# Optimization experiments

Measured on AMD Instinct MI355X. Metric: run time of the kernel, lower is better.

Reference implementation:

```python
import jax, jax.numpy as jnp
import numpy as np

D_MODEL = 512
NHEAD = 8


def setup_inputs() -> dict:
    key = jax.random.key(0)
    ks = jax.random.split(key, 8)
    d = D_MODEL
    low_feats = jax.random.normal(ks[0], (1, d, 32, 32), dtype=jnp.float32)
    guide_feats = jax.random.normal(ks[1], (1, d, 128, 128), dtype=jnp.float32)
    s = 1.0 / np.sqrt(d)
    Wq = jax.random.normal(ks[2], (d, d), dtype=jnp.float32) * s
    Wk = jax.random.normal(ks[3], (d, d), dtype=jnp.float32) * s
    Wv = jax.random.normal(ks[4], (d, d), dtype=jnp.float32) * s
    Wm = jax.random.normal(ks[5], (d, d), dtype=jnp.float32) * s
    gamma = jnp.ones((d,), dtype=jnp.float32)
    beta = jnp.zeros((d,), dtype=jnp.float32)
    return {"low_feats": low_feats, "guide_feats": guide_feats, "Wq": Wq,
            "Wk": Wk, "Wv": Wv, "Wm": Wm, "gamma": gamma, "beta": beta}


def _gather_windows(feat_hw, H, W):
    # feat_hw: [b, h, w, nhead, dim]. For each guide pixel (Y,X), nearest low
    # pixel is (Y*h//H, X*w//W) (PyTorch 'nearest'); gather its 3x3 neighborhood
    # with replicate padding (index clamping). Window order = ky*3+kx, matching
    # F.unfold channel layout. Returns [b, H*W, 9, nhead, dim].
    b, h, w, nh, dm = feat_hw.shape
    offs = jnp.array([-1, 0, 1])
    y0 = jnp.arange(H) * h // H                      # [H]
    x0 = jnp.arange(W) * w // W                      # [W]
    ys = jnp.clip(y0[:, None] + offs, 0, h - 1)      # [H,3] (ky)
    xs = jnp.clip(x0[:, None] + offs, 0, w - 1)      # [W,3] (kx)
    # -> [b, H, W, 3(ky), 3(kx), nhead, dim]
    g = feat_hw[:, ys[:, None, :, None], xs[None, :, None, :]]
    return g.reshape(b, H * W, 9, nh, dm)


def reference(low_feats, guide_feats, Wq, Wk, Wv, Wm, gamma, beta):
    b, d, H, W = guide_feats.shape
    _, _, h, w = low_feats.shape
    nh = NHEAD
    dm = d // nh
    g = guide_feats.transpose(0, 2, 3, 1).reshape(b, H * W, d)
    l = low_feats.transpose(0, 2, 3, 1).reshape(b, h * w, d)
    q = (g @ Wq.T).reshape(b, H * W, nh, dm)                 # [b,N,h,d]
    K = (l @ Wk.T).reshape(b, h, w, nh, dm)
    V = (l @ Wv.T).reshape(b, h, w, nh, dm)
    key = _gather_windows(K, H, W)                           # [b,N,9,h,d]
    val = _gather_windows(V, H, W)
    scale = 1.0 / jnp.sqrt(jnp.asarray(dm, dtype=q.dtype))
    # (q/sqrt(dm)) @ (k/sqrt(dm)) * sqrt(dm) == q@k / sqrt(dm)
    score = jnp.einsum('bnhd,bnkhd->bnhk', q, key) * scale
    attn = jax.nn.softmax(score, axis=-1)
    msg = jnp.einsum('bnhk,bnkhd->bnhd', attn, val).reshape(b, H * W, d)
    msg = msg @ Wm.T
    # LayerNorm(d_model), eps=1e-5
    mu = jnp.mean(msg, axis=-1, keepdims=True)
    var = jnp.mean((msg - mu) ** 2, axis=-1, keepdims=True)
    msg = (msg - mu) * jax.lax.rsqrt(var + 1e-5) * gamma + beta
    return msg.transpose(0, 2, 1).reshape(b, d, H, W)
```

## Files before the change

### kernel.cpp

```cpp
#include <hip/hip_runtime.h>
#include <hip/hip_bf16.h>
#include <stdint.h>

#define NQ 16384
#define NL 1024
#define DM 512

typedef __bf16 bf16_t;
typedef __bf16 bf16x8 __attribute__((ext_vector_type(8)));
typedef __bf16 bf16x4 __attribute__((ext_vector_type(4)));
typedef float f32x4 __attribute__((ext_vector_type(4)));

__device__ __forceinline__ void gload_lds16(const void* g, void* l) {
  __builtin_amdgcn_global_load_lds(
      (const __attribute__((address_space(1))) uint32_t*)g,
      (__attribute__((address_space(3))) uint32_t*)l, 16, 0, 0);
}

__global__ __launch_bounds__(256) void cvt_transpose(const float* __restrict__ src,
                                                     bf16_t* __restrict__ dst, int ncols) {
  __shared__ float tl[32][33];
  const int n0 = blockIdx.x * 32, c0 = blockIdx.y * 32;
  const int t = threadIdx.x, c = t & 31, r = t >> 5;
#pragma unroll
  for (int it = 0; it < 4; ++it) {
    int rr = r + it * 8;
    tl[rr][c] = src[(size_t)(c0 + rr) * ncols + n0 + c];
  }
  __syncthreads();
#pragma unroll
  for (int it = 0; it < 4; ++it) {
    int rr = r + it * 8;
    dst[(size_t)(n0 + rr) * 512 + c0 + c] = (bf16_t)tl[c][rr];
  }
}

__global__ __launch_bounds__(256) void cvt_w(const float* __restrict__ s0, const float* __restrict__ s1,
                                             const float* __restrict__ s2, const float* __restrict__ s3,
                                             bf16_t* __restrict__ d0, bf16_t* __restrict__ d1,
                                             bf16_t* __restrict__ d2, bf16_t* __restrict__ d3) {
  const float* s;
  bf16_t* d;
  switch (blockIdx.y) {
    case 0: s = s0; d = d0; break;
    case 1: s = s1; d = d1; break;
    case 2: s = s2; d = d2; break;
    default: s = s3; d = d3; break;
  }
  const int i = (blockIdx.x * 256 + threadIdx.x) * 4;
  float4 v = *(const float4*)(s + i);
  bf16x4 o = {(bf16_t)v.x, (bf16_t)v.y, (bf16_t)v.z, (bf16_t)v.w};
  *(bf16x4*)(d + i) = o;
}

template <typename OutT>
__global__ __launch_bounds__(256) void gemm_bt(const bf16_t* __restrict__ A,
                                               const bf16_t* __restrict__ B,
                                               OutT* __restrict__ C, int M, int N, int K) {
  __shared__ __align__(16) bf16_t As[128 * 64];
  __shared__ __align__(16) bf16_t Bs[128 * 64];
  const int t = threadIdx.x;
  const int lane = t & 63;
  const int wave = t >> 6;
  const int wr = (wave >> 1) * 64;
  const int wc = (wave & 1) * 64;
  const int bm = blockIdx.x * 128;
  const int bn = blockIdx.y * 128;
  const int r0 = t >> 3;
  const int c0 = (t & 7) * 8;
  f32x4 acc[4][4] = {};
  for (int k0 = 0; k0 < K; k0 += 64) {
#pragma unroll
    for (int it = 0; it < 4; ++it) {
      const int r = r0 + it * 32;
      gload_lds16(A + (size_t)(bm + r) * K + k0 + c0, &As[r * 64 + c0]);
      gload_lds16(B + (size_t)(bn + r) * K + k0 + c0, &Bs[r * 64 + c0]);
    }
    __syncthreads();
#pragma unroll
    for (int kk = 0; kk < 2; ++kk) {
      bf16x8 af[4], bfv[4];
#pragma unroll
      for (int i = 0; i < 4; ++i)
        af[i] = *(const bf16x8*)&As[(wr + i * 16 + (lane & 15)) * 64 + kk * 32 + (lane >> 4) * 8];
#pragma unroll
      for (int i = 0; i < 4; ++i)
        bfv[i] = *(const bf16x8*)&Bs[(wc + i * 16 + (lane & 15)) * 64 + kk * 32 + (lane >> 4) * 8];
#pragma unroll
      for (int i = 0; i < 4; ++i)
#pragma unroll
        for (int j = 0; j < 4; ++j)
          acc[i][j] = __builtin_amdgcn_mfma_f32_16x16x32_bf16(af[i], bfv[j], acc[i][j], 0, 0, 0);
    }
    __syncthreads();
  }
  const int crow = bm + wr + ((lane >> 4) * 4);
  const int ccol = bn + wc + (lane & 15);
#pragma unroll
  for (int i = 0; i < 4; ++i)
#pragma unroll
    for (int j = 0; j < 4; ++j) {
      const int row = crow + i * 16;
      const int col = ccol + j * 16;
#pragma unroll
      for (int v = 0; v < 4; ++v)
        C[(size_t)(row + v) * N + col] = (OutT)acc[i][j][v];
    }
}

__global__ __launch_bounds__(128) void attn_win(const bf16_t* __restrict__ Q,
                                                const bf16_t* __restrict__ Kb,
                                                const bf16_t* __restrict__ Vb,
                                                bf16_t* __restrict__ Msg) {
  __shared__ __align__(16) bf16_t Kl[9 * 512];
  __shared__ __align__(16) bf16_t Vl[9 * 512];
  const int t = threadIdx.x;
  const int lane = t & 63;
  const int wave = t >> 6;
  const int tile = blockIdx.x;
  const int ty = tile >> 5, tx = tile & 31;
  for (int kk = wave; kk < 9; kk += 2) {
    int ky = kk / 3, kx = kk - ky * 3;
    int yy = min(max(ty - 1 + ky, 0), 31);
    int xx = min(max(tx - 1 + kx, 0), 31);
    size_t p = (size_t)(yy * 32 + xx) * 512;
    int dst = kk * 512 + (lane & 7) * 64 + (lane >> 3) * 8;
    *(bf16x8*)&Kl[dst] = *(const bf16x8*)&Kb[p + lane * 8];
    *(bf16x8*)&Vl[dst] = *(const bf16x8*)&Vb[p + lane * 8];
  }
  __syncthreads();
  const int pl = t >> 3, h = t & 7;
  const int y = ty * 4 + (pl >> 2), x = tx * 4 + (pl & 3);
  const size_t n = (size_t)y * 128 + x;
  const bf16_t* qrow = Q + n * 512 + h * 64;
  float s[9] = {};
#pragma unroll
  for (int i8 = 0; i8 < 8; ++i8) {
    bf16x8 q8 = *(const bf16x8*)(qrow + i8 * 8);
#pragma unroll
    for (int k = 0; k < 9; ++k) {
      bf16x8 k8 = *(const bf16x8*)&Kl[k * 512 + i8 * 64 + h * 8];
#pragma unroll
      for (int e = 0; e < 8; ++e) s[k] += (float)q8[e] * (float)k8[e];
    }
  }
  float mx = s[0];
#pragma unroll
  for (int k = 1; k < 9; ++k) mx = fmaxf(mx, s[k]);
  float sum = 0.f;
#pragma unroll
  for (int k = 0; k < 9; ++k) {
    s[k] = __expf((s[k] - mx) * 0.125f);
    sum += s[k];
  }
  const float inv = 1.0f / sum;
#pragma unroll
  for (int k = 0; k < 9; ++k) s[k] *= inv;
  bf16_t* orow = Msg + n * 512 + h * 64;
#pragma unroll
  for (int i8 = 0; i8 < 8; ++i8) {
    float accv[8] = {};
#pragma unroll
    for (int k = 0; k < 9; ++k) {
      bf16x8 v8 = *(const bf16x8*)&Vl[k * 512 + i8 * 64 + h * 8];
#pragma unroll
      for (int e = 0; e < 8; ++e) accv[e] += s[k] * (float)v8[e];
    }
    bf16x8 o;
#pragma unroll
    for (int e = 0; e < 8; ++e) o[e] = (bf16_t)accv[e];
    *(bf16x8*)&orow[i8 * 8] = o;
  }
}

__global__ __launch_bounds__(256) void ln_stats(const float* __restrict__ P, float2* __restrict__ stats) {
  const int row = blockIdx.x * 4 + (threadIdx.x >> 6);
  const int lane = threadIdx.x & 63;
  const float4* p = (const float4*)(P + (size_t)row * 512);
  float s = 0.f, s2 = 0.f;
#pragma unroll
  for (int i = 0; i < 2; ++i) {
    float4 v = p[lane + i * 64];
    s += v.x + v.y + v.z + v.w;
    s2 += v.x * v.x + v.y * v.y + v.z * v.z + v.w * v.w;
  }
#pragma unroll
  for (int off = 32; off > 0; off >>= 1) {
    s += __shfl_down(s, off);
    s2 += __shfl_down(s2, off);
  }
  if (lane == 0) {
    float mu = s * (1.f / 512.f);
    float var = s2 * (1.f / 512.f) - mu * mu;
    stats[row] = make_float2(mu, rsqrtf(var + 1e-5f));
  }
}

__global__ __launch_bounds__(256) void ln_transpose(const float* __restrict__ P,
                                                    const float2* __restrict__ stats,
                                                    const float* __restrict__ gamma,
                                                    const float* __restrict__ beta,
                                                    float* __restrict__ out) {
  __shared__ float tl[32][33];
  __shared__ float2 st[32];
  const int n0 = blockIdx.x * 32, j0 = blockIdx.y * 32;
  const int t = threadIdx.x, c = t & 31, r = t >> 5;
  if (t < 32) st[t] = stats[n0 + t];
  __syncthreads();
  const float g = gamma[j0 + c], b = beta[j0 + c];
#pragma unroll
  for (int it = 0; it < 4; ++it) {
    int rr = r + it * 8;
    float v = P[(size_t)(n0 + rr) * 512 + j0 + c];
    float2 ms = st[rr];
    tl[rr][c] = (v - ms.x) * ms.y * g + b;
  }
  __syncthreads();
#pragma unroll
  for (int it = 0; it < 4; ++it) {
    int rr = r + it * 8;
    out[(size_t)(j0 + rr) * NQ + n0 + c] = tl[c][rr];
  }
}

extern "C" void kernel_launch(void* const* d_in, const int* in_sizes, int n_in,
                              void* d_out, int out_size, void* d_ws, size_t ws_size,
                              hipStream_t stream) {
  const float* low = (const float*)d_in[0];
  const float* guide = (const float*)d_in[1];
  const float* Wq = (const float*)d_in[2];
  const float* Wk = (const float*)d_in[3];
  const float* Wv = (const float*)d_in[4];
  const float* Wm = (const float*)d_in[5];
  const float* gamma = (const float*)d_in[6];
  const float* beta = (const float*)d_in[7];
  float* out = (float*)d_out;

  char* w = (char*)d_ws;
  bf16_t* Gbf = (bf16_t*)w; w += (size_t)NQ * 512 * 2;
  bf16_t* Lbf = (bf16_t*)w; w += (size_t)NL * 512 * 2;
  bf16_t* Wqb = (bf16_t*)w; w += (size_t)512 * 512 * 2;
  bf16_t* Wkb = (bf16_t*)w; w += (size_t)512 * 512 * 2;
  bf16_t* Wvb = (bf16_t*)w; w += (size_t)512 * 512 * 2;
  bf16_t* Wmb = (bf16_t*)w; w += (size_t)512 * 512 * 2;
  bf16_t* Qbf = (bf16_t*)w; w += (size_t)NQ * 512 * 2;
  bf16_t* Kbf = (bf16_t*)w; w += (size_t)NL * 512 * 2;
  bf16_t* Vbf = (bf16_t*)w; w += (size_t)NL * 512 * 2;
  bf16_t* Msg = (bf16_t*)w; w += (size_t)NQ * 512 * 2;
  float* Pf = (float*)w;    w += (size_t)NQ * 512 * 4;
  float2* stats = (float2*)w;

  cvt_transpose<<<dim3(NQ / 32, 16), 256, 0, stream>>>(guide, Gbf, NQ);
  cvt_transpose<<<dim3(NL / 32, 16), 256, 0, stream>>>(low, Lbf, NL);
  cvt_w<<<dim3(256, 4), 256, 0, stream>>>(Wq, Wk, Wv, Wm, Wqb, Wkb, Wvb, Wmb);
  gemm_bt<bf16_t><<<dim3(NQ / 128, 4), 256, 0, stream>>>(Gbf, Wqb, Qbf, NQ, 512, 512);
  gemm_bt<bf16_t><<<dim3(NL / 128, 4), 256, 0, stream>>>(Lbf, Wkb, Kbf, NL, 512, 512);
  gemm_bt<bf16_t><<<dim3(NL / 128, 4), 256, 0, stream>>>(Lbf, Wvb, Vbf, NL, 512, 512);
  attn_win<<<dim3(1024), 128, 0, stream>>>(Qbf, Kbf, Vbf, Msg);
  gemm_bt<float><<<dim3(NQ / 128, 4), 256, 0, stream>>>(Msg, Wmb, Pf, NQ, 512, 512);
  ln_stats<<<dim3(NQ / 4), 256, 0, stream>>>(Pf, stats);
  ln_transpose<<<dim3(NQ / 32, 512 / 32), 256, 0, stream>>>(Pf, stats, gamma, beta, out);
}
```

Before: 196.2 us.

## Fuse output GEMM with LayerNorm and transpose, merge QKV and conversion launches

The output projection GEMM now computes a full 64x512 row tile per block, stages it in LDS, computes LayerNorm statistics in-register and writes the normalized, transposed result directly. This removes the fp32 intermediate round trip and two extra kernels. The Q/K/V GEMMs are merged into one launch with a concatenated K|V weight, and the two input transposes are merged into one launch. The trade-offs are large LDS use (about 131KB per block) and only 256 blocks for the fused GEMM, which may limit occupancy.

```diff
diff --git a/kernel.cpp b/kernel.cpp
--- a/kernel.cpp
+++ b/kernel.cpp
@@ -4,7 +4,6 @@
 
 #define NQ 16384
 #define NL 1024
-#define DM 512
 
 typedef __bf16 bf16_t;
 typedef __bf16 bf16x8 __attribute__((ext_vector_type(8)));
@@ -17,10 +16,17 @@
       (__attribute__((address_space(3))) uint32_t*)l, 16, 0, 0);
 }
 
-__global__ __launch_bounds__(256) void cvt_transpose(const float* __restrict__ src,
-                                                     bf16_t* __restrict__ dst, int ncols) {
+__global__ __launch_bounds__(256) void cvt_transpose_all(const float* __restrict__ guide,
+                                                         const float* __restrict__ low,
+                                                         bf16_t* __restrict__ Gbf,
+                                                         bf16_t* __restrict__ Lbf) {
   __shared__ float tl[32][33];
-  const int n0 = blockIdx.x * 32, c0 = blockIdx.y * 32;
+  const float* src;
+  bf16_t* dst;
+  int ncols, n0;
+  if (blockIdx.x < 512) { src = guide; dst = Gbf; ncols = NQ; n0 = blockIdx.x * 32; }
+  else                  { src = low;   dst = Lbf; ncols = NL; n0 = (blockIdx.x - 512) * 32; }
+  const int c0 = blockIdx.y * 32;
   const int t = threadIdx.x, c = t & 31, r = t >> 5;
 #pragma unroll
   for (int it = 0; it < 4; ++it) {
@@ -53,28 +59,34 @@
   *(bf16x4*)(d + i) = o;
 }
 
-template <typename OutT>
-__global__ __launch_bounds__(256) void gemm_bt(const bf16_t* __restrict__ A,
-                                               const bf16_t* __restrict__ B,
-                                               OutT* __restrict__ C, int M, int N, int K) {
+__global__ __launch_bounds__(256) void gemm_qkv(const bf16_t* __restrict__ G,
+                                                const bf16_t* __restrict__ Wq,
+                                                bf16_t* __restrict__ Qo,
+                                                const bf16_t* __restrict__ L,
+                                                const bf16_t* __restrict__ Wkv,
+                                                bf16_t* __restrict__ KVo) {
   __shared__ __align__(16) bf16_t As[128 * 64];
   __shared__ __align__(16) bf16_t Bs[128 * 64];
+  const bf16_t *A, *B;
+  bf16_t* C;
+  int N, bm, bn;
+  const int bid = blockIdx.x;
+  if (bid < 512) { A = G; B = Wq; C = Qo; N = 512; bm = (bid >> 2) * 128; bn = (bid & 3) * 128; }
+  else { int id = bid - 512; A = L; B = Wkv; C = KVo; N = 1024; bm = (id >> 3) * 128; bn = (id & 7) * 128; }
   const int t = threadIdx.x;
   const int lane = t & 63;
   const int wave = t >> 6;
   const int wr = (wave >> 1) * 64;
   const int wc = (wave & 1) * 64;
-  const int bm = blockIdx.x * 128;
-  const int bn = blockIdx.y * 128;
   const int r0 = t >> 3;
   const int c0 = (t & 7) * 8;
   f32x4 acc[4][4] = {};
-  for (int k0 = 0; k0 < K; k0 += 64) {
+  for (int k0 = 0; k0 < 512; k0 += 64) {
 #pragma unroll
     for (int it = 0; it < 4; ++it) {
       const int r = r0 + it * 32;
-      gload_lds16(A + (size_t)(bm + r) * K + k0 + c0, &As[r * 64 + c0]);
-      gload_lds16(B + (size_t)(bn + r) * K + k0 + c0, &Bs[r * 64 + c0]);
+      gload_lds16(A + (size_t)(bm + r) * 512 + k0 + c0, &As[r * 64 + c0]);
+      gload_lds16(B + (size_t)(bn + r) * 512 + k0 + c0, &Bs[r * 64 + c0]);
     }
     __syncthreads();
 #pragma unroll
@@ -104,13 +116,12 @@
       const int col = ccol + j * 16;
 #pragma unroll
       for (int v = 0; v < 4; ++v)
-        C[(size_t)(row + v) * N + col] = (OutT)acc[i][j][v];
+        C[(size_t)(row + v) * N + col] = (bf16_t)acc[i][j][v];
     }
 }
 
 __global__ __launch_bounds__(128) void attn_win(const bf16_t* __restrict__ Q,
-                                                const bf16_t* __restrict__ Kb,
-                                                const bf16_t* __restrict__ Vb,
+                                                const bf16_t* __restrict__ KV,
                                                 bf16_t* __restrict__ Msg) {
   __shared__ __align__(16) bf16_t Kl[9 * 512];
   __shared__ __align__(16) bf16_t Vl[9 * 512];
@@ -123,10 +134,10 @@
     int ky = kk / 3, kx = kk - ky * 3;
     int yy = min(max(ty - 1 + ky, 0), 31);
     int xx = min(max(tx - 1 + kx, 0), 31);
-    size_t p = (size_t)(yy * 32 + xx) * 512;
+    size_t p = (size_t)(yy * 32 + xx) * 1024;
     int dst = kk * 512 + (lane & 7) * 64 + (lane >> 3) * 8;
-    *(bf16x8*)&Kl[dst] = *(const bf16x8*)&Kb[p + lane * 8];
-    *(bf16x8*)&Vl[dst] = *(const bf16x8*)&Vb[p + lane * 8];
+    *(bf16x8*)&Kl[dst] = *(const bf16x8*)&KV[p + lane * 8];
+    *(bf16x8*)&Vl[dst] = *(const bf16x8*)&KV[p + 512 + lane * 8];
   }
   __syncthreads();
   const int pl = t >> 3, h = t & 7;
@@ -173,53 +184,100 @@
   }
 }
 
-__global__ __launch_bounds__(256) void ln_stats(const float* __restrict__ P, float2* __restrict__ stats) {
-  const int row = blockIdx.x * 4 + (threadIdx.x >> 6);
-  const int lane = threadIdx.x & 63;
-  const float4* p = (const float4*)(P + (size_t)row * 512);
-  float s = 0.f, s2 = 0.f;
-#pragma unroll
-  for (int i = 0; i < 2; ++i) {
-    float4 v = p[lane + i * 64];
-    s += v.x + v.y + v.z + v.w;
-    s2 += v.x * v.x + v.y * v.y + v.z * v.z + v.w * v.w;
-  }
-#pragma unroll
-  for (int off = 32; off > 0; off >>= 1) {
-    s += __shfl_down(s, off);
-    s2 += __shfl_down(s2, off);
-  }
-  if (lane == 0) {
+__global__ __launch_bounds__(512) void gemm_ln_out(const bf16_t* __restrict__ A,
+                                                   const bf16_t* __restrict__ B,
+                                                   const float* __restrict__ gamma,
+                                                   const float* __restrict__ beta,
+                                                   float* __restrict__ out) {
+  __shared__ __align__(16) char smem[64 * 513 * 4];
+  __shared__ float2 part[64][4];
+  __shared__ float2 st[64];
+  bf16_t* As = (bf16_t*)smem;
+  bf16_t* Bs = (bf16_t*)(smem + 8192);
+  float* Cl = (float*)smem;
+  const int t = threadIdx.x;
+  const int lane = t & 63;
+  const int wave = t >> 6;
+  const int wr = (wave >> 2) * 32;
+  const int wc = (wave & 3) * 128;
+  const int bm = blockIdx.x * 64;
+  const int sr = t >> 3;
+  const int sc = (t & 7) * 8;
+  f32x4 acc[2][8] = {};
+  for (int k0 = 0; k0 < 512; k0 += 64) {
+    gload_lds16(A + (size_t)(bm + sr) * 512 + k0 + sc, &As[sr * 64 + sc]);
+#pragma unroll
+    for (int it = 0; it < 8; ++it) {
+      const int r = sr + it * 64;
+      gload_lds16(B + (size_t)r * 512 + k0 + sc, &Bs[r * 64 + sc]);
+    }
+    __syncthreads();
+#pragma unroll
+    for (int kk = 0; kk < 2; ++kk) {
+      bf16x8 af[2], bfv[8];
+#pragma unroll
+      for (int i = 0; i < 2; ++i)
+        af[i] = *(const bf16x8*)&As[(wr + i * 16 + (lane & 15)) * 64 + kk * 32 + (lane >> 4) * 8];
+#pragma unroll
+      for (int j = 0; j < 8; ++j)
+        bfv[j] = *(const bf16x8*)&Bs[(wc + j * 16 + (lane & 15)) * 64 + kk * 32 + (lane >> 4) * 8];
+#pragma unroll
+      for (int i = 0; i < 2; ++i)
+#pragma unroll
+        for (int j = 0; j < 8; ++j)
+          acc[i][j] = __builtin_amdgcn_mfma_f32_16x16x32_bf16(af[i], bfv[j], acc[i][j], 0, 0, 0);
+    }
+    __syncthreads();
+  }
+#pragma unroll
+  for (int i = 0; i < 2; ++i)
+#pragma unroll
+    for (int j = 0; j < 8; ++j) {
+      const int row = wr + i * 16 + (lane >> 4) * 4;
+      const int col = wc + j * 16 + (lane & 15);
+#pragma unroll
+      for (int v = 0; v < 4; ++v) Cl[(row + v) * 513 + col] = acc[i][j][v];
+    }
+#pragma unroll
+  for (int i = 0; i < 2; ++i)
+#pragma unroll
+    for (int v = 0; v < 4; ++v) {
+      float s = 0.f, s2 = 0.f;
+#pragma unroll
+      for (int j = 0; j < 8; ++j) {
+        float x = acc[i][j][v];
+        s += x;
+        s2 += x * x;
+      }
+#pragma unroll
+      for (int m = 1; m < 16; m <<= 1) {
+        s += __shfl_xor(s, m, 64);
+        s2 += __shfl_xor(s2, m, 64);
+      }
+      if ((lane & 15) == 0) {
+        const int row = wr + i * 16 + (lane >> 4) * 4 + v;
+        part[row][wave & 3] = make_float2(s, s2);
+      }
+    }
+  __syncthreads();
+  if (t < 64) {
+    float2 p0 = part[t][0], p1 = part[t][1], p2 = part[t][2], p3 = part[t][3];
+    float s = p0.x + p1.x + p2.x + p3.x;
+    float s2 = p0.y + p1.y + p2.y + p3.y;
     float mu = s * (1.f / 512.f);
     float var = s2 * (1.f / 512.f) - mu * mu;
-    stats[row] = make_float2(mu, rsqrtf(var + 1e-5f));
-  }
-}
-
-__global__ __launch_bounds__(256) void ln_transpose(const float* __restrict__ P,
-                                                    const float2* __restrict__ stats,
-                                                    const float* __restrict__ gamma,
-                                                    const float* __restrict__ beta,
-                                                    float* __restrict__ out) {
-  __shared__ float tl[32][33];
-  __shared__ float2 st[32];
-  const int n0 = blockIdx.x * 32, j0 = blockIdx.y * 32;
-  const int t = threadIdx.x, c = t & 31, r = t >> 5;
-  if (t < 32) st[t] = stats[n0 + t];
+    st[t] = make_float2(mu, rsqrtf(var + 1e-5f));
+  }
   __syncthreads();
-  const float g = gamma[j0 + c], b = beta[j0 + c];
-#pragma unroll
-  for (int it = 0; it < 4; ++it) {
-    int rr = r + it * 8;
-    float v = P[(size_t)(n0 + rr) * 512 + j0 + c];
-    float2 ms = st[rr];
-    tl[rr][c] = (v - ms.x) * ms.y * g + b;
-  }
-  __syncthreads();
-#pragma unroll
-  for (int it = 0; it < 4; ++it) {
-    int rr = r + it * 8;
-    out[(size_t)(j0 + rr) * NQ + n0 + c] = tl[c][rr];
+  const int n = t & 63;
+  const int j0 = t >> 6;
+  const float2 ms = st[n];
+#pragma unroll 8
+  for (int jj = 0; jj < 64; ++jj) {
+    const int j = j0 * 64 + jj;
+    const float g = gamma[j], b = beta[j];
+    const float x = Cl[n * 513 + j];
+    out[(size_t)j * NQ + bm + n] = (x - ms.x) * ms.y * g + b;
   }
 }
 
@@ -240,24 +298,15 @@
   bf16_t* Gbf = (bf16_t*)w; w += (size_t)NQ * 512 * 2;
   bf16_t* Lbf = (bf16_t*)w; w += (size_t)NL * 512 * 2;
   bf16_t* Wqb = (bf16_t*)w; w += (size_t)512 * 512 * 2;
-  bf16_t* Wkb = (bf16_t*)w; w += (size_t)512 * 512 * 2;
-  bf16_t* Wvb = (bf16_t*)w; w += (size_t)512 * 512 * 2;
+  bf16_t* Wkvb = (bf16_t*)w; w += (size_t)1024 * 512 * 2;
   bf16_t* Wmb = (bf16_t*)w; w += (size_t)512 * 512 * 2;
   bf16_t* Qbf = (bf16_t*)w; w += (size_t)NQ * 512 * 2;
-  bf16_t* Kbf = (bf16_t*)w; w += (size_t)NL * 512 * 2;
-  bf16_t* Vbf = (bf16_t*)w; w += (size_t)NL * 512 * 2;
+  bf16_t* KVbf = (bf16_t*)w; w += (size_t)NL * 1024 * 2;
   bf16_t* Msg = (bf16_t*)w; w += (size_t)NQ * 512 * 2;
-  float* Pf = (float*)w;    w += (size_t)NQ * 512 * 4;
-  float2* stats = (float2*)w;
-
-  cvt_transpose<<<dim3(NQ / 32, 16), 256, 0, stream>>>(guide, Gbf, NQ);
-  cvt_transpose<<<dim3(NL / 32, 16), 256, 0, stream>>>(low, Lbf, NL);
-  cvt_w<<<dim3(256, 4), 256, 0, stream>>>(Wq, Wk, Wv, Wm, Wqb, Wkb, Wvb, Wmb);
-  gemm_bt<bf16_t><<<dim3(NQ / 128, 4), 256, 0, stream>>>(Gbf, Wqb, Qbf, NQ, 512, 512);
-  gemm_bt<bf16_t><<<dim3(NL / 128, 4), 256, 0, stream>>>(Lbf, Wkb, Kbf, NL, 512, 512);
-  gemm_bt<bf16_t><<<dim3(NL / 128, 4), 256, 0, stream>>>(Lbf, Wvb, Vbf, NL, 512, 512);
-  attn_win<<<dim3(1024), 128, 0, stream>>>(Qbf, Kbf, Vbf, Msg);
-  gemm_bt<float><<<dim3(NQ / 128, 4), 256, 0, stream>>>(Msg, Wmb, Pf, NQ, 512, 512);
-  ln_stats<<<dim3(NQ / 4), 256, 0, stream>>>(Pf, stats);
-  ln_transpose<<<dim3(NQ / 32, 512 / 32), 256, 0, stream>>>(Pf, stats, gamma, beta, out);
-}
+
+  cvt_transpose_all<<<dim3(544, 16), 256, 0, stream>>>(guide, low, Gbf, Lbf);
+  cvt_w<<<dim3(256, 4), 256, 0, stream>>>(Wq, Wk, Wv, Wm, Wqb, Wkvb, Wkvb + (size_t)512 * 512, Wmb);
+  gemm_qkv<<<dim3(576), 256, 0, stream>>>(Gbf, Wqb, Qbf, Lbf, Wkvb, KVbf);
+  attn_win<<<dim3(1024), 128, 0, stream>>>(Qbf, KVbf, Msg);
+  gemm_ln_out<<<dim3(NQ / 64), 512, 0, stream>>>(Msg, Wmb, gamma, beta, out);
+}
```

Measured after the change: 174.5 us. 11.0% less time.
